# Kernel tuning notes

Measured on AMD Instinct MI355X. Metric: run time of the kernel, lower is better.

## Reference

```python
import jax, jax.numpy as jnp
import numpy as np

DIM = 768
HEADS = 12
DIM_HEAD = 64
INNER = HEADS * DIM_HEAD  # 768
B, N = 8, 1024
SCALE = DIM_HEAD ** -0.5


def setup_inputs() -> dict:
    key = jax.random.key(0)
    ks = jax.random.split(key, 8)
    std = 0.02
    x = jax.random.normal(ks[0], (B, N, DIM), dtype=jnp.float32)
    W_q = jax.random.normal(ks[1], (DIM, INNER), dtype=jnp.float32) * std
    W_kv = jax.random.normal(ks[2], (DIM, 2 * INNER), dtype=jnp.float32) * std
    mix_pre = jax.random.normal(ks[3], (HEADS, HEADS), dtype=jnp.float32)
    mix_post = jax.random.normal(ks[4], (HEADS, HEADS), dtype=jnp.float32)
    W_out = jax.random.normal(ks[5], (INNER, DIM), dtype=jnp.float32) * std
    b_out = jnp.zeros((DIM,), dtype=jnp.float32)
    return {"x": x, "W_q": W_q, "W_kv": W_kv, "mix_pre": mix_pre,
            "mix_post": mix_post, "W_out": W_out, "b_out": b_out}


def reference(x, W_q, W_kv, mix_pre, mix_post, W_out, b_out):
    b, n, _ = x.shape
    # projections (context == x since no cross-attn context given)
    q = x @ W_q                                   # (b, n, inner)
    kv = x @ W_kv                                 # (b, n, 2*inner)
    k, v = jnp.split(kv, 2, axis=-1)
    # (b, n, h*d) -> (b, h, n, d)
    split_heads = lambda t: t.reshape(b, n, HEADS, DIM_HEAD).transpose(0, 2, 1, 3)
    q, k, v = split_heads(q), split_heads(k), split_heads(v)
    dots = jnp.einsum('bhid,bhjd->bhij', q, k) * SCALE
    dots = jnp.einsum('bhij,hg->bgij', dots, mix_pre)    # pre-softmax talking heads
    attn = jax.nn.softmax(dots, axis=-1)
    attn = jnp.einsum('bhij,hg->bgij', attn, mix_post)   # post-softmax talking heads
    out = jnp.einsum('bhij,bhjd->bhid', attn, v)         # (b, h, n, d)
    out = out.transpose(0, 2, 1, 3).reshape(b, n, INNER)
    return out @ W_out + b_out
```

## Files before the change

kernel.cpp:

```cpp
#include <hip/hip_runtime.h>
#include <hip/hip_bf16.h>

typedef __attribute__((ext_vector_type(8))) short short8_t;
typedef __attribute__((ext_vector_type(8))) unsigned short ushort8_t;
typedef __attribute__((ext_vector_type(4))) float f32x4;

#define SCALE 0.125f

__device__ __forceinline__ unsigned short f32_to_bf16_rne(float f) {
  unsigned int u = __float_as_uint(f);
  unsigned int r = 0x7FFFu + ((u >> 16) & 1u);
  return (unsigned short)((u + r) >> 16);
}

__device__ __forceinline__ int swz(int i) { return (i + (i >> 2)) & 3; }

__global__ __launch_bounds__(256) void cast_x_kernel(const float4* __restrict__ in,
                                                     ushort4* __restrict__ out, int n4) {
  int i = blockIdx.x * 256 + threadIdx.x;
  if (i < n4) {
    float4 v = in[i];
    ushort4 o;
    o.x = f32_to_bf16_rne(v.x); o.y = f32_to_bf16_rne(v.y);
    o.z = f32_to_bf16_rne(v.z); o.w = f32_to_bf16_rne(v.w);
    out[i] = o;
  }
}

__global__ __launch_bounds__(256) void transpose_cast_kernel(const float* __restrict__ in,
                                                             unsigned short* __restrict__ out,
                                                             int R, int C) {
  __shared__ float tile[32][33];
  int c0 = blockIdx.x * 32, r0 = blockIdx.y * 32;
  int tx = threadIdx.x & 31, ty = threadIdx.x >> 5;
  #pragma unroll
  for (int i = ty; i < 32; i += 8)
    tile[i][tx] = in[(long)(r0 + i) * C + c0 + tx];
  __syncthreads();
  #pragma unroll
  for (int i = ty; i < 32; i += 8)
    out[(long)(c0 + i) * R + r0 + tx] = f32_to_bf16_rne(tile[tx][i]);
}

__global__ __launch_bounds__(256) void transpose_v_kernel(const unsigned short* __restrict__ KV,
                                                          unsigned short* __restrict__ Vt) {
  __shared__ unsigned short tile[64][72];
  const int j0 = blockIdx.x * 64, h = blockIdx.y, b = blockIdx.z;
  const int tid = threadIdx.x;
  for (int c = tid; c < 512; c += 256) {
    int j = c >> 3, dp = (c & 7) * 8;
    *(ushort8_t*)&tile[j][dp] =
        *(const ushort8_t*)&KV[(long)(b * 1024 + j0 + j) * 1536 + 768 + h * 64 + dp];
  }
  __syncthreads();
  for (int c = tid; c < 512; c += 256) {
    int d = c >> 3, jp = (c & 7) * 8;
    ushort8_t v;
    #pragma unroll
    for (int t = 0; t < 8; t++) v[t] = tile[jp + t][d];
    int jg = j0 + jp;
    int jt_ = jg >> 5;
    int u = (jg >> 3) & 3;
    *(ushort8_t*)&Vt[((long)(b * 12 + h) * 64 + d) * 1024 + (jt_ << 5) + ((u ^ swz(d)) << 3)] = v;
  }
}

template <int BM, int BN, bool OUT_F32, bool BIAS, bool SUM2>
__global__ __launch_bounds__(256) void gemm_nt(const unsigned short* __restrict__ A,
                                               const unsigned short* __restrict__ A2, int lda,
                                               const unsigned short* __restrict__ B, int ldb,
                                               void* __restrict__ Cv, int ldc,
                                               const float* __restrict__ bias,
                                               int M, int N, int K) {
  constexpr int BK = 32;
  constexpr int LDT = BK + 8;
  __shared__ unsigned short As[BM][LDT];
  __shared__ unsigned short Bs[BN][LDT];
  const int m0 = blockIdx.y * BM;
  const int n0 = blockIdx.x * BN;
  const int tid = threadIdx.x;
  const int lane = tid & 63;
  const int w = tid >> 6;
  constexpr int WM = BM / 2, WN = BN / 2;
  constexpr int FM = WM / 16, FN = WN / 16;
  const int wr = w >> 1, wc = w & 1;

  f32x4 acc[FM][FN];
  #pragma unroll
  for (int a = 0; a < FM; a++)
    #pragma unroll
    for (int b2 = 0; b2 < FN; b2++) acc[a][b2] = (f32x4){0.f, 0.f, 0.f, 0.f};

  const int rl = lane & 15;
  const int kq = (lane >> 4) * 8;

  for (int k0 = 0; k0 < K; k0 += BK) {
    __syncthreads();
    for (int c = tid; c < BM * (BK / 8); c += 256) {
      int row = c >> 2, kp = (c & 3) * 8;
      ushort8_t v = *(const ushort8_t*)&A[(long)(m0 + row) * lda + k0 + kp];
      if (SUM2) {
        ushort8_t v2 = *(const ushort8_t*)&A2[(long)(m0 + row) * lda + k0 + kp];
        #pragma unroll
        for (int x = 0; x < 8; ++x)
          v[x] = f32_to_bf16_rne(__uint_as_float((unsigned)v[x] << 16) +
                                 __uint_as_float((unsigned)v2[x] << 16));
      }
      *(ushort8_t*)&As[row][kp] = v;
    }
    for (int c = tid; c < BN * (BK / 8); c += 256) {
      int row = c >> 2, kp = (c & 3) * 8;
      *(ushort8_t*)&Bs[row][kp] = *(const ushort8_t*)&B[(long)(n0 + row) * ldb + k0 + kp];
    }
    __syncthreads();
    short8_t af[FM], bfr[FN];
    #pragma unroll
    for (int fm = 0; fm < FM; fm++) af[fm] = *(const short8_t*)&As[wr * WM + fm * 16 + rl][kq];
    #pragma unroll
    for (int fn = 0; fn < FN; fn++) bfr[fn] = *(const short8_t*)&Bs[wc * WN + fn * 16 + rl][kq];
    #pragma unroll
    for (int fm = 0; fm < FM; fm++)
      #pragma unroll
      for (int fn = 0; fn < FN; fn++)
        acc[fm][fn] = __builtin_amdgcn_mfma_f32_16x16x32_bf16(af[fm], bfr[fn], acc[fm][fn], 0, 0, 0);
  }

  const int rq4 = (lane >> 4) * 4;
  #pragma unroll
  for (int fm = 0; fm < FM; fm++)
    #pragma unroll
    for (int fn = 0; fn < FN; fn++)
      #pragma unroll
      for (int j = 0; j < 4; j++) {
        int row = m0 + wr * WM + fm * 16 + rq4 + j;
        int col = n0 + wc * WN + fn * 16 + rl;
        float v = acc[fm][fn][j];
        if (BIAS) v += bias[col];
        if (OUT_F32)
          ((float*)Cv)[(long)row * ldc + col] = v;
        else
          ((unsigned short*)Cv)[(long)row * ldc + col] = f32_to_bf16_rne(v);
      }
}

__global__ __launch_bounds__(256, 1) void qk_mix_exp_kernel(
    const unsigned short* __restrict__ Qb, const unsigned short* __restrict__ KVb,
    const float* __restrict__ mix_pre,
    unsigned short* __restrict__ Eo, float* __restrict__ Lpart, int b_base) {
  __shared__ unsigned short Dbuf[12 * 32 * 44];
  __shared__ float mpre_s[144];
  const int jt = blockIdx.x, it2 = blockIdx.y, zc = blockIdx.z;
  const int b = b_base + zc;
  const int tid = threadIdx.x, lane = tid & 63, w = tid >> 6;
  const int r15 = lane & 15, q = lane >> 4;
  if (tid < 144) mpre_s[tid] = mix_pre[tid] * SCALE;

  const int isel = w >> 1, jsel = w & 1;
  const long qrow = (long)(b * 1024 + it2 * 32 + isel * 16 + r15) * 768 + q * 8;
  const long krow = (long)(b * 1024 + jt * 32 + jsel * 16 + r15) * 1536 + q * 8;
  const int jcol = jsel * 16 + r15;
  for (int h = 0; h < 12; ++h) {
    const int kb = h * 64;
    short8_t a0 = *(const short8_t*)&Qb[qrow + kb];
    short8_t a1 = *(const short8_t*)&Qb[qrow + kb + 32];
    short8_t b0 = *(const short8_t*)&KVb[krow + kb];
    short8_t b1 = *(const short8_t*)&KVb[krow + kb + 32];
    f32x4 h0 = {0.f, 0.f, 0.f, 0.f};
    h0 = __builtin_amdgcn_mfma_f32_16x16x32_bf16(a0, b0, h0, 0, 0, 0);
    h0 = __builtin_amdgcn_mfma_f32_16x16x32_bf16(a1, b1, h0, 0, 0, 0);
    #pragma unroll
    for (int e = 0; e < 4; ++e) {
      int il = isel * 16 + q * 4 + e;
      Dbuf[h * 1408 + il * 44 + jcol] = f32_to_bf16_rne(h0[e]);
    }
  }
  __syncthreads();

  const int i_loc = tid >> 3;
  const int jg = tid & 7;
  const int r = i_loc & 15;
  const long chunkbase = ((long)((zc * 32 + jt) * 64) + it2 * 2 + (i_loc >> 4)) * 6144;
  const int eslot = r * 32 + ((((jg >> 1) ^ swz(r))) << 3) + (jg & 1) * 4;

  float dvf[12][4];
  #pragma unroll
  for (int h = 0; h < 12; ++h) {
    ushort4 dv = *(const ushort4*)&Dbuf[h * 1408 + i_loc * 44 + jg * 4];
    dvf[h][0] = __uint_as_float((unsigned)dv.x << 16);
    dvf[h][1] = __uint_as_float((unsigned)dv.y << 16);
    dvf[h][2] = __uint_as_float((unsigned)dv.z << 16);
    dvf[h][3] = __uint_as_float((unsigned)dv.w << 16);
  }

  #pragma unroll
  for (int g = 0; g < 12; ++g) {
    float a0 = 0.f, a1 = 0.f, a2 = 0.f, a3 = 0.f;
    #pragma unroll
    for (int h = 0; h < 12; ++h) {
      const float wgt = mpre_s[h * 12 + g];
      a0 += wgt * dvf[h][0]; a1 += wgt * dvf[h][1];
      a2 += wgt * dvf[h][2]; a3 += wgt * dvf[h][3];
    }
    a0 = __expf(a0); a1 = __expf(a1); a2 = __expf(a2); a3 = __expf(a3);
    float s = a0 + a1 + a2 + a3;
    s += __shfl_xor(s, 1);
    s += __shfl_xor(s, 2);
    s += __shfl_xor(s, 4);
    if (jg == (g & 7))
      Lpart[((long)(zc * 32 + jt) * 12 + g) * 1024 + it2 * 32 + i_loc] = s;
    ushort4 ev;
    ev.x = f32_to_bf16_rne(a0); ev.y = f32_to_bf16_rne(a1);
    ev.z = f32_to_bf16_rne(a2); ev.w = f32_to_bf16_rne(a3);
    *(ushort4*)&Eo[chunkbase + g * 512 + eslot] = ev;
  }
}

__global__ __launch_bounds__(256) void lsum_kernel(const float* __restrict__ Lpart,
                                                   float* __restrict__ invl, int nb) {
  int id = blockIdx.x * 256 + threadIdx.x;
  if (id >= nb * 12288) return;
  int z = id / 12288, r = id - z * 12288;
  float s = 0.f;
  #pragma unroll 4
  for (int jt = 0; jt < 32; ++jt) s += Lpart[((long)(z * 32 + jt)) * 12288 + r];
  invl[id] = 1.f / s;
}

__global__ __launch_bounds__(256, 1) void pv2_kernel(
    const unsigned short* __restrict__ E, const unsigned short* __restrict__ Vt,
    const float* __restrict__ invl, const float* __restrict__ mix_post,
    unsigned short* __restrict__ AOp0, unsigned short* __restrict__ AOp1, int b_base) {
  __shared__ unsigned short Ebuf[6144];
  __shared__ unsigned short Vbuf[24576];
  __shared__ unsigned short Pbuf[6144];
  const int it = blockIdx.x, jh = blockIdx.y, zc = blockIdx.z;
  const int b = b_base + zc;
  const int tid = threadIdx.x, lane = tid & 63, w = tid >> 6;
  const int r15 = lane & 15, q = lane >> 4;
  const int i_loc = tid & 15, jslot = (tid >> 4) & 3;

  float W2[3][12];
  #pragma unroll
  for (int g = 0; g < 12; ++g) {
    float il = invl[(zc * 12 + g) * 1024 + it * 16 + i_loc];
    #pragma unroll
    for (int r = 0; r < 3; ++r) W2[r][g] = mix_post[g * 12 + w * 3 + r] * il;
  }

  f32x4 acc[3][4];
  #pragma unroll
  for (int gl = 0; gl < 3; ++gl)
    #pragma unroll
    for (int df = 0; df < 4; ++df) acc[gl][df] = (f32x4){0.f, 0.f, 0.f, 0.f};

  const long vbase = (long)(b * 12) * 64 * 1024;
  ushort8_t ereg[3], vreg[12];
  auto loadE = [&](int jt) {
    const long cbs = ((long)((zc * 32 + jt) * 16 + (it >> 2))) * 24576 + (it & 3) * 6144;
    #pragma unroll
    for (int u = 0; u < 3; ++u)
      ereg[u] = *(const ushort8_t*)&E[cbs + (u * 256 + tid) * 8];
  };
  auto loadV = [&](int jt) {
    #pragma unroll
    for (int u = 0; u < 12; ++u) {
      int unit = u * 256 + tid;
      vreg[u] = *(const ushort8_t*)&Vt[vbase + (long)(unit >> 2) * 1024 + jt * 32 +
                                       ((unit & 3) << 3)];
    }
  };
  const int jt0 = jh * 16;
  loadE(jt0);
  loadV(jt0);

  for (int t = 0; t < 16; ++t) {
    __syncthreads();
    #pragma unroll
    for (int u = 0; u < 3; ++u) *(ushort8_t*)&Ebuf[(u * 256 + tid) * 8] = ereg[u];
    #pragma unroll
    for (int u = 0; u < 12; ++u) *(ushort8_t*)&Vbuf[(u * 256 + tid) * 8] = vreg[u];
    __syncthreads();
    if (t < 15) { loadE(jt0 + t + 1); loadV(jt0 + t + 1); }

    float p[3][8];
    #pragma unroll
    for (int r = 0; r < 3; ++r)
      #pragma unroll
      for (int jj = 0; jj < 8; ++jj) p[r][jj] = 0.f;
    const int esl = (jslot ^ swz(i_loc)) << 3;
    #pragma unroll
    for (int g = 0; g < 12; ++g) {
      ushort8_t ev = *(const ushort8_t*)&Ebuf[g * 512 + i_loc * 32 + esl];
      #pragma unroll
      for (int jj = 0; jj < 8; ++jj) {
        float ef = __uint_as_float((unsigned)ev[jj] << 16);
        #pragma unroll
        for (int r = 0; r < 3; ++r) p[r][jj] += W2[r][g] * ef;
      }
    }
    #pragma unroll
    for (int r = 0; r < 3; ++r) {
      ushort8_t pv;
      #pragma unroll
      for (int jj = 0; jj < 8; ++jj) pv[jj] = f32_to_bf16_rne(p[r][jj]);
      *(ushort8_t*)&Pbuf[(w * 3 + r) * 512 + i_loc * 32 + esl] = pv;
    }
    __syncthreads();

    #pragma unroll
    for (int gl = 0; gl < 3; ++gl) {
      const int g2 = w * 3 + gl;
      short8_t af = *(const short8_t*)&Pbuf[g2 * 512 + r15 * 32 + ((q ^ swz(r15)) << 3)];
      #pragma unroll
      for (int df = 0; df < 4; ++df) {
        short8_t bf = *(const short8_t*)&Vbuf[(g2 * 64 + df * 16 + r15) * 32 +
                                              ((q ^ swz(r15)) << 3)];
        acc[gl][df] = __builtin_amdgcn_mfma_f32_16x16x32_bf16(af, bf, acc[gl][df], 0, 0, 0);
      }
    }
  }

  unsigned short* AOp = jh ? AOp1 : AOp0;
  #pragma unroll
  for (int gl = 0; gl < 3; ++gl) {
    const int g2 = w * 3 + gl;
    #pragma unroll
    for (int df = 0; df < 4; ++df)
      #pragma unroll
      for (int e = 0; e < 4; ++e) {
        int row = it * 16 + q * 4 + e;
        int col = g2 * 64 + df * 16 + r15;
        AOp[(long)(b * 1024 + row) * 768 + col] = f32_to_bf16_rne(acc[gl][df][e]);
      }
  }
}

extern "C" void kernel_launch(void* const* d_in, const int* in_sizes, int n_in,
                              void* d_out, int out_size, void* d_ws, size_t ws_size,
                              hipStream_t stream) {
  const float* x        = (const float*)d_in[0];
  const float* W_q      = (const float*)d_in[1];
  const float* W_kv     = (const float*)d_in[2];
  const float* mix_pre  = (const float*)d_in[3];
  const float* mix_post = (const float*)d_in[4];
  const float* W_out    = (const float*)d_in[5];
  const float* b_out    = (const float*)d_in[6];
  float* out = (float*)d_out;

  char* p = (char*)d_ws;
  auto alloc = [&](size_t bytes) { char* r = p; p += (bytes + 255) & ~(size_t)255; return r; };
  unsigned short* xb    = (unsigned short*)alloc(8192ull * 768 * 2);
  unsigned short* WqT   = (unsigned short*)alloc(768ull * 768 * 2);
  unsigned short* WkvT  = (unsigned short*)alloc(1536ull * 768 * 2);
  unsigned short* WoutT = (unsigned short*)alloc(768ull * 768 * 2);
  unsigned short* Qb    = (unsigned short*)alloc(8192ull * 768 * 2);
  unsigned short* KVb   = (unsigned short*)alloc(8192ull * 1536 * 2);
  unsigned short* Vt    = (unsigned short*)alloc(8ull * 12 * 64 * 1024 * 2);
  unsigned short* AOp0  = (unsigned short*)alloc(8192ull * 768 * 2);
  unsigned short* AOp1  = (unsigned short*)alloc(8192ull * 768 * 2);

  const int nz = (ws_size >= 322000000ull) ? 8 : (ws_size >= 211000000ull) ? 4 : 2;
  unsigned short* E     = (unsigned short*)alloc((size_t)nz * 32 * 16 * 24576 * 2);
  float*          Lpart = (float*)alloc((size_t)nz * 32 * 12 * 1024 * 4);
  float*          invl  = (float*)alloc((size_t)nz * 12 * 1024 * 4);

  cast_x_kernel<<<6144, 256, 0, stream>>>((const float4*)x, (ushort4*)xb, 8192 * 768 / 4);
  transpose_cast_kernel<<<dim3(24, 24), 256, 0, stream>>>(W_q, WqT, 768, 768);
  transpose_cast_kernel<<<dim3(48, 24), 256, 0, stream>>>(W_kv, WkvT, 768, 1536);
  transpose_cast_kernel<<<dim3(24, 24), 256, 0, stream>>>(W_out, WoutT, 768, 768);

  gemm_nt<128, 128, false, false, false><<<dim3(6, 64), 256, 0, stream>>>(
      xb, nullptr, 768, WqT, 768, Qb, 768, nullptr, 8192, 768, 768);
  gemm_nt<128, 128, false, false, false><<<dim3(12, 64), 256, 0, stream>>>(
      xb, nullptr, 768, WkvT, 768, KVb, 1536, nullptr, 8192, 1536, 768);

  transpose_v_kernel<<<dim3(16, 12, 8), 256, 0, stream>>>(KVb, Vt);

  for (int b0 = 0; b0 < 8; b0 += nz) {
    qk_mix_exp_kernel<<<dim3(32, 32, nz), 256, 0, stream>>>(Qb, KVb, mix_pre, E, Lpart, b0);
    lsum_kernel<<<nz * 48, 256, 0, stream>>>(Lpart, invl, nz);
    pv2_kernel<<<dim3(64, 2, nz), 256, 0, stream>>>(E, Vt, invl, mix_post, AOp0, AOp1, b0);
  }

  gemm_nt<128, 128, true, true, true><<<dim3(6, 64), 256, 0, stream>>>(
      AOp0, AOp1, 768, WoutT, 768, out, 768, b_out, 8192, 768, 768);
}
```

Measured before the change: 487.7 us.

## Recompute QK scores in PV kernel instead of materializing exp matrix

The first attention pass now only computes the per-row softmax denominators and no longer writes the bf16 exponentiated score tensor E to global memory. The PV kernel recomputes QK^T, the pre-mix and exp for each tile on the fly, scales by the inverse sums, applies the post-mix and multiplies by V, which it now reads directly from global instead of staging it through registers and LDS. This removes the large E write/read traffic and the batch-chunked loop over workspace size, so every batch runs in a single launch. In exchange the QK matmul and exp are done twice, the PV kernel loses its software prefetch and gains extra syncs, and V is read from global with no LDS reuse.

```diff
diff --git a/kernel.cpp b/kernel.cpp
--- a/kernel.cpp
+++ b/kernel.cpp
@@ -12,7 +12,9 @@
   unsigned int r = 0x7FFFu + ((u >> 16) & 1u);
   return (unsigned short)((u + r) >> 16);
 }
-
+__device__ __forceinline__ float bf16_to_f32(unsigned short s) {
+  return __uint_as_float((unsigned)s << 16);
+}
 __device__ __forceinline__ int swz(int i) { return (i + (i >> 2)) & 3; }
 
 __global__ __launch_bounds__(256) void cast_x_kernel(const float4* __restrict__ in,
@@ -58,10 +60,7 @@
     ushort8_t v;
     #pragma unroll
     for (int t = 0; t < 8; t++) v[t] = tile[jp + t][d];
-    int jg = j0 + jp;
-    int jt_ = jg >> 5;
-    int u = (jg >> 3) & 3;
-    *(ushort8_t*)&Vt[((long)(b * 12 + h) * 64 + d) * 1024 + (jt_ << 5) + ((u ^ swz(d)) << 3)] = v;
+    *(ushort8_t*)&Vt[((long)(b * 12 + h) * 64 + d) * 1024 + j0 + jp] = v;
   }
 }
 
@@ -103,8 +102,7 @@
         ushort8_t v2 = *(const ushort8_t*)&A2[(long)(m0 + row) * lda + k0 + kp];
         #pragma unroll
         for (int x = 0; x < 8; ++x)
-          v[x] = f32_to_bf16_rne(__uint_as_float((unsigned)v[x] << 16) +
-                                 __uint_as_float((unsigned)v2[x] << 16));
+          v[x] = f32_to_bf16_rne(bf16_to_f32(v[x]) + bf16_to_f32(v2[x]));
       }
       *(ushort8_t*)&As[row][kp] = v;
     }
@@ -143,17 +141,19 @@
       }
 }
 
-__global__ __launch_bounds__(256, 1) void qk_mix_exp_kernel(
+__global__ __launch_bounds__(256, 1) void qk_sum_kernel(
     const unsigned short* __restrict__ Qb, const unsigned short* __restrict__ KVb,
-    const float* __restrict__ mix_pre,
-    unsigned short* __restrict__ Eo, float* __restrict__ Lpart, int b_base) {
+    const float* __restrict__ mix_pre, float* __restrict__ Lpart) {
   __shared__ unsigned short Dbuf[12 * 32 * 44];
-  __shared__ float mpre_s[144];
+  __shared__ float mpre_t[144];
   const int jt = blockIdx.x, it2 = blockIdx.y, zc = blockIdx.z;
-  const int b = b_base + zc;
+  const int b = zc;
   const int tid = threadIdx.x, lane = tid & 63, w = tid >> 6;
   const int r15 = lane & 15, q = lane >> 4;
-  if (tid < 144) mpre_s[tid] = mix_pre[tid] * SCALE;
+  if (tid < 144) {
+    int g = tid / 12, h = tid - g * 12;
+    mpre_t[tid] = mix_pre[h * 12 + g] * SCALE;
+  }
 
   const int isel = w >> 1, jsel = w & 1;
   const long qrow = (long)(b * 1024 + it2 * 32 + isel * 16 + r15) * 768 + q * 8;
@@ -178,18 +178,13 @@
 
   const int i_loc = tid >> 3;
   const int jg = tid & 7;
-  const int r = i_loc & 15;
-  const long chunkbase = ((long)((zc * 32 + jt) * 64) + it2 * 2 + (i_loc >> 4)) * 6144;
-  const int eslot = r * 32 + ((((jg >> 1) ^ swz(r))) << 3) + (jg & 1) * 4;
 
   float dvf[12][4];
   #pragma unroll
   for (int h = 0; h < 12; ++h) {
     ushort4 dv = *(const ushort4*)&Dbuf[h * 1408 + i_loc * 44 + jg * 4];
-    dvf[h][0] = __uint_as_float((unsigned)dv.x << 16);
-    dvf[h][1] = __uint_as_float((unsigned)dv.y << 16);
-    dvf[h][2] = __uint_as_float((unsigned)dv.z << 16);
-    dvf[h][3] = __uint_as_float((unsigned)dv.w << 16);
+    dvf[h][0] = bf16_to_f32(dv.x); dvf[h][1] = bf16_to_f32(dv.y);
+    dvf[h][2] = bf16_to_f32(dv.z); dvf[h][3] = bf16_to_f32(dv.w);
   }
 
   #pragma unroll
@@ -197,7 +192,7 @@
     float a0 = 0.f, a1 = 0.f, a2 = 0.f, a3 = 0.f;
     #pragma unroll
     for (int h = 0; h < 12; ++h) {
-      const float wgt = mpre_s[h * 12 + g];
+      const float wgt = mpre_t[g * 12 + h];
       a0 += wgt * dvf[h][0]; a1 += wgt * dvf[h][1];
       a2 += wgt * dvf[h][2]; a3 += wgt * dvf[h][3];
     }
@@ -208,10 +203,6 @@
     s += __shfl_xor(s, 4);
     if (jg == (g & 7))
       Lpart[((long)(zc * 32 + jt) * 12 + g) * 1024 + it2 * 32 + i_loc] = s;
-    ushort4 ev;
-    ev.x = f32_to_bf16_rne(a0); ev.y = f32_to_bf16_rne(a1);
-    ev.z = f32_to_bf16_rne(a2); ev.w = f32_to_bf16_rne(a3);
-    *(ushort4*)&Eo[chunkbase + g * 512 + eslot] = ev;
   }
 }
 
@@ -226,26 +217,45 @@
   invl[id] = 1.f / s;
 }
 
-__global__ __launch_bounds__(256, 1) void pv2_kernel(
-    const unsigned short* __restrict__ E, const unsigned short* __restrict__ Vt,
-    const float* __restrict__ invl, const float* __restrict__ mix_post,
-    unsigned short* __restrict__ AOp0, unsigned short* __restrict__ AOp1, int b_base) {
-  __shared__ unsigned short Ebuf[6144];
-  __shared__ unsigned short Vbuf[24576];
-  __shared__ unsigned short Pbuf[6144];
+__global__ __launch_bounds__(256, 1) void fused_pv_kernel(
+    const unsigned short* __restrict__ Qb, const unsigned short* __restrict__ KVb,
+    const unsigned short* __restrict__ Vt, const float* __restrict__ invl,
+    const float* __restrict__ mix_pre, const float* __restrict__ mix_post,
+    unsigned short* __restrict__ AOp0, unsigned short* __restrict__ AOp1) {
+  __shared__ unsigned short Dbuf[12][16][34];
+  __shared__ unsigned short Ebuf[12][16][40];
+  __shared__ unsigned short Pbuf[12 * 512];
+  __shared__ float mpre_t[144];
   const int it = blockIdx.x, jh = blockIdx.y, zc = blockIdx.z;
-  const int b = b_base + zc;
+  const int b = zc;
   const int tid = threadIdx.x, lane = tid & 63, w = tid >> 6;
   const int r15 = lane & 15, q = lane >> 4;
-  const int i_loc = tid & 15, jslot = (tid >> 4) & 3;
-
-  float W2[3][12];
-  #pragma unroll
-  for (int g = 0; g < 12; ++g) {
-    float il = invl[(zc * 12 + g) * 1024 + it * 16 + i_loc];
-    #pragma unroll
-    for (int r = 0; r < 3; ++r) W2[r][g] = mix_post[g * 12 + w * 3 + r] * il;
-  }
+  if (tid < 144) {
+    int g = tid / 12, h = tid - g * 12;
+    mpre_t[tid] = mix_pre[h * 12 + g] * SCALE;
+  }
+
+  const int h0 = w * 3;
+  const long qbase = (long)(b * 1024 + it * 16 + r15) * 768;
+  short8_t qf[3][2];
+  #pragma unroll
+  for (int hh = 0; hh < 3; ++hh) {
+    qf[hh][0] = *(const short8_t*)&Qb[qbase + (h0 + hh) * 64 + q * 8];
+    qf[hh][1] = *(const short8_t*)&Qb[qbase + (h0 + hh) * 64 + 32 + q * 8];
+  }
+
+  float wpost[3][12];
+  #pragma unroll
+  for (int g = 0; g < 12; ++g)
+    #pragma unroll
+    for (int r = 0; r < 3; ++r) wpost[r][g] = mix_post[g * 12 + w * 3 + r];
+
+  const int i_mix = tid & 15;
+  const int jp = tid >> 4;
+  const int jslot = (tid >> 4) & 3;
+  float il[12];
+  #pragma unroll
+  for (int g = 0; g < 12; ++g) il[g] = invl[(zc * 12 + g) * 1024 + it * 16 + i_mix];
 
   f32x4 acc[3][4];
   #pragma unroll
@@ -254,56 +264,77 @@
     for (int df = 0; df < 4; ++df) acc[gl][df] = (f32x4){0.f, 0.f, 0.f, 0.f};
 
   const long vbase = (long)(b * 12) * 64 * 1024;
-  ushort8_t ereg[3], vreg[12];
-  auto loadE = [&](int jt) {
-    const long cbs = ((long)((zc * 32 + jt) * 16 + (it >> 2))) * 24576 + (it & 3) * 6144;
-    #pragma unroll
-    for (int u = 0; u < 3; ++u)
-      ereg[u] = *(const ushort8_t*)&E[cbs + (u * 256 + tid) * 8];
-  };
-  auto loadV = [&](int jt) {
-    #pragma unroll
-    for (int u = 0; u < 12; ++u) {
-      int unit = u * 256 + tid;
-      vreg[u] = *(const ushort8_t*)&Vt[vbase + (long)(unit >> 2) * 1024 + jt * 32 +
-                                       ((unit & 3) << 3)];
-    }
-  };
-  const int jt0 = jh * 16;
-  loadE(jt0);
-  loadV(jt0);
 
   for (int t = 0; t < 16; ++t) {
+    const int j0 = (jh * 16 + t) * 32;
+
+    #pragma unroll
+    for (int hh = 0; hh < 3; ++hh) {
+      #pragma unroll
+      for (int jhf = 0; jhf < 2; ++jhf) {
+        const long kr = (long)(b * 1024 + j0 + jhf * 16 + r15) * 1536 + (h0 + hh) * 64 + q * 8;
+        short8_t b0 = *(const short8_t*)&KVb[kr];
+        short8_t b1 = *(const short8_t*)&KVb[kr + 32];
+        f32x4 d = {0.f, 0.f, 0.f, 0.f};
+        d = __builtin_amdgcn_mfma_f32_16x16x32_bf16(qf[hh][0], b0, d, 0, 0, 0);
+        d = __builtin_amdgcn_mfma_f32_16x16x32_bf16(qf[hh][1], b1, d, 0, 0, 0);
+        #pragma unroll
+        for (int e = 0; e < 4; ++e)
+          Dbuf[h0 + hh][q * 4 + e][jhf * 16 + r15] = f32_to_bf16_rne(d[e]);
+      }
+    }
     __syncthreads();
-    #pragma unroll
-    for (int u = 0; u < 3; ++u) *(ushort8_t*)&Ebuf[(u * 256 + tid) * 8] = ereg[u];
-    #pragma unroll
-    for (int u = 0; u < 12; ++u) *(ushort8_t*)&Vbuf[(u * 256 + tid) * 8] = vreg[u];
+
+    {
+      float dv0[12], dv1[12];
+      #pragma unroll
+      for (int h = 0; h < 12; ++h) {
+        ushort2 dp = *(const ushort2*)&Dbuf[h][i_mix][jp * 2];
+        dv0[h] = bf16_to_f32(dp.x);
+        dv1[h] = bf16_to_f32(dp.y);
+      }
+      #pragma unroll
+      for (int g = 0; g < 12; ++g) {
+        float m0 = 0.f, m1 = 0.f;
+        #pragma unroll
+        for (int h = 0; h < 12; ++h) {
+          const float wgt = mpre_t[g * 12 + h];
+          m0 += wgt * dv0[h]; m1 += wgt * dv1[h];
+        }
+        m0 = __expf(m0) * il[g];
+        m1 = __expf(m1) * il[g];
+        ushort2 ev;
+        ev.x = f32_to_bf16_rne(m0);
+        ev.y = f32_to_bf16_rne(m1);
+        *(ushort2*)&Ebuf[g][i_mix][jp * 2] = ev;
+      }
+    }
     __syncthreads();
-    if (t < 15) { loadE(jt0 + t + 1); loadV(jt0 + t + 1); }
-
-    float p[3][8];
-    #pragma unroll
-    for (int r = 0; r < 3; ++r)
-      #pragma unroll
-      for (int jj = 0; jj < 8; ++jj) p[r][jj] = 0.f;
-    const int esl = (jslot ^ swz(i_loc)) << 3;
-    #pragma unroll
-    for (int g = 0; g < 12; ++g) {
-      ushort8_t ev = *(const ushort8_t*)&Ebuf[g * 512 + i_loc * 32 + esl];
-      #pragma unroll
-      for (int jj = 0; jj < 8; ++jj) {
-        float ef = __uint_as_float((unsigned)ev[jj] << 16);
-        #pragma unroll
-        for (int r = 0; r < 3; ++r) p[r][jj] += W2[r][g] * ef;
-      }
-    }
-    #pragma unroll
-    for (int r = 0; r < 3; ++r) {
-      ushort8_t pv;
-      #pragma unroll
-      for (int jj = 0; jj < 8; ++jj) pv[jj] = f32_to_bf16_rne(p[r][jj]);
-      *(ushort8_t*)&Pbuf[(w * 3 + r) * 512 + i_loc * 32 + esl] = pv;
+
+    {
+      float p[3][8];
+      #pragma unroll
+      for (int r = 0; r < 3; ++r)
+        #pragma unroll
+        for (int jj = 0; jj < 8; ++jj) p[r][jj] = 0.f;
+      #pragma unroll
+      for (int g = 0; g < 12; ++g) {
+        ushort8_t ev = *(const ushort8_t*)&Ebuf[g][i_mix][jslot * 8];
+        #pragma unroll
+        for (int jj = 0; jj < 8; ++jj) {
+          float ef = bf16_to_f32(ev[jj]);
+          p[0][jj] += wpost[0][g] * ef;
+          p[1][jj] += wpost[1][g] * ef;
+          p[2][jj] += wpost[2][g] * ef;
+        }
+      }
+      #pragma unroll
+      for (int r = 0; r < 3; ++r) {
+        ushort8_t pv;
+        #pragma unroll
+        for (int jj = 0; jj < 8; ++jj) pv[jj] = f32_to_bf16_rne(p[r][jj]);
+        *(ushort8_t*)&Pbuf[(w * 3 + r) * 512 + i_mix * 32 + ((jslot ^ swz(i_mix)) << 3)] = pv;
+      }
     }
     __syncthreads();
 
@@ -313,9 +344,9 @@
       short8_t af = *(const short8_t*)&Pbuf[g2 * 512 + r15 * 32 + ((q ^ swz(r15)) << 3)];
       #pragma unroll
       for (int df = 0; df < 4; ++df) {
-        short8_t bf = *(const short8_t*)&Vbuf[(g2 * 64 + df * 16 + r15) * 32 +
-                                              ((q ^ swz(r15)) << 3)];
-        acc[gl][df] = __builtin_amdgcn_mfma_f32_16x16x32_bf16(af, bf, acc[gl][df], 0, 0, 0);
+        short8_t bv = *(const short8_t*)&Vt[vbase + (long)(g2 * 64 + df * 16 + r15) * 1024 +
+                                            j0 + q * 8];
+        acc[gl][df] = __builtin_amdgcn_mfma_f32_16x16x32_bf16(af, bv, acc[gl][df], 0, 0, 0);
       }
     }
   }
@@ -358,11 +389,8 @@
   unsigned short* Vt    = (unsigned short*)alloc(8ull * 12 * 64 * 1024 * 2);
   unsigned short* AOp0  = (unsigned short*)alloc(8192ull * 768 * 2);
   unsigned short* AOp1  = (unsigned short*)alloc(8192ull * 768 * 2);
-
-  const int nz = (ws_size >= 322000000ull) ? 8 : (ws_size >= 211000000ull) ? 4 : 2;
-  unsigned short* E     = (unsigned short*)alloc((size_t)nz * 32 * 16 * 24576 * 2);
-  float*          Lpart = (float*)alloc((size_t)nz * 32 * 12 * 1024 * 4);
-  float*          invl  = (float*)alloc((size_t)nz * 12 * 1024 * 4);
+  float*          Lpart = (float*)alloc(8ull * 32 * 12 * 1024 * 4);
+  float*          invl  = (float*)alloc(8ull * 12 * 1024 * 4);
 
   cast_x_kernel<<<6144, 256, 0, stream>>>((const float4*)x, (ushort4*)xb, 8192 * 768 / 4);
   transpose_cast_kernel<<<dim3(24, 24), 256, 0, stream>>>(W_q, WqT, 768, 768);
@@ -376,11 +404,10 @@
 
   transpose_v_kernel<<<dim3(16, 12, 8), 256, 0, stream>>>(KVb, Vt);
 
-  for (int b0 = 0; b0 < 8; b0 += nz) {
-    qk_mix_exp_kernel<<<dim3(32, 32, nz), 256, 0, stream>>>(Qb, KVb, mix_pre, E, Lpart, b0);
-    lsum_kernel<<<nz * 48, 256, 0, stream>>>(Lpart, invl, nz);
-    pv2_kernel<<<dim3(64, 2, nz), 256, 0, stream>>>(E, Vt, invl, mix_post, AOp0, AOp1, b0);
-  }
+  qk_sum_kernel<<<dim3(32, 32, 8), 256, 0, stream>>>(Qb, KVb, mix_pre, Lpart);
+  lsum_kernel<<<384, 256, 0, stream>>>(Lpart, invl, 8);
+  fused_pv_kernel<<<dim3(64, 2, 8), 256, 0, stream>>>(Qb, KVb, Vt, invl, mix_pre, mix_post,
+                                                      AOp0, AOp1);
 
   gemm_nt<128, 128, true, true, true><<<dim3(6, 64), 256, 0, stream>>>(
       AOp0, AOp1, 768, WoutT, 768, out, 768, b_out, 8192, 768, 768);
```

Result: slower. 849.4 us (+74.1%).
